# Optimization experiments

Measured on AMD Instinct MI355X. Metric: run time of the kernel, lower is better.

## Reference

```python
import jax, jax.numpy as jnp
import numpy as np

N, E, F, H, G, C, L = 50000, 800000, 128, 256, 128, 10, 3


def _gcn(x, src, dst, norm, W, b, n):
    # PyG GCNConv: h = x W; out_i = sum_{j->i} norm_ji h_j (+ self loops already in src/dst); + bias
    h = x @ W
    msg = h[src] * norm[:, None]              # [E+N, H]
    return jax.ops.segment_sum(msg, dst, num_segments=n) + b


def setup_inputs() -> dict:
    key = jax.random.key(0)
    ks = jax.random.split(key, 8)
    x = jax.random.normal(ks[0], (N, F), dtype=jnp.float32)
    edge_index = jax.random.randint(ks[1], (2, E), 0, N, dtype=jnp.int32)
    batch = jnp.sort(jax.random.randint(ks[2], (N,), 0, G, dtype=jnp.int32))
    graph_hidden = jax.random.normal(ks[3], (G, H), dtype=jnp.float32)
    W0 = jax.random.normal(ks[4], (F, H), dtype=jnp.float32) / np.sqrt(F)
    b0 = jnp.zeros((H,), jnp.float32)
    Ws = jax.random.normal(ks[5], (L, H, H), dtype=jnp.float32) / np.sqrt(H)
    bs = jnp.zeros((L, H), jnp.float32)
    Wlin = jax.random.normal(ks[6], (H, C), dtype=jnp.float32) / np.sqrt(H)
    blin = jnp.zeros((C,), jnp.float32)
    return {"x": x, "edge_index": edge_index, "batch": batch, "graph_hidden": graph_hidden,
            "W0": W0, "b0": b0, "Ws": Ws, "bs": bs, "Wlin": Wlin, "blin": blin}


def reference(x, edge_index, batch, graph_hidden, W0, b0, Ws, bs, Wlin, blin):
    n = x.shape[0]
    loops = jnp.arange(n, dtype=edge_index.dtype)
    src = jnp.concatenate([edge_index[0], loops])   # self loops appended
    dst = jnp.concatenate([edge_index[1], loops])
    deg = jax.ops.segment_sum(jnp.ones_like(src, dtype=x.dtype), dst, num_segments=n)
    inv_sqrt = jnp.where(deg > 0, jax.lax.rsqrt(deg), 0.0)
    norm = inv_sqrt[src] * inv_sqrt[dst]            # [E+N]

    h = _gcn(x, src, dst, norm, W0, b0, n)          # to_hidden (no activation, matches source)
    res = jax.lax.stop_gradient(graph_hidden[batch])  # no_grad residual, vectorized
    for i in range(Ws.shape[0]):
        h = h + res
        h = jax.nn.relu(_gcn(h, src, dst, norm, Ws[i], bs[i], n))
        # dropout is identity in eval mode

    counts = jax.ops.segment_sum(jnp.ones((n,), x.dtype), batch, num_segments=G)
    gm = jax.ops.segment_sum(h, batch, num_segments=G) / jnp.maximum(counts, 1.0)[:, None]
    gm = gm + graph_hidden
    y = gm @ Wlin + blin
    return (y, gm)
```

## Files before the change

kernel.cpp:

```cpp
#include <hip/hip_runtime.h>


typedef float f32x4 __attribute__((ext_vector_type(4)));
typedef float f32x2 __attribute__((ext_vector_type(2)));

__device__ inline float bf2f(unsigned short u) {
  union { unsigned int i; float f; } v;
  v.i = (unsigned int)u << 16;
  return v.f;
}
__device__ inline unsigned short f2bf(float f) {
  union { unsigned int i; float f; } v;
  v.f = f;
  unsigned int i = v.i;
  return (unsigned short)((i + 0x7fffu + ((i >> 16) & 1u)) >> 16);
}
__device__ inline unsigned pack4_fp8(float a, float b, float c, float d) {
  int r = 0;
  r = __builtin_amdgcn_cvt_pk_fp8_f32(a, b, r, false);
  r = __builtin_amdgcn_cvt_pk_fp8_f32(c, d, r, true);
  return (unsigned)r;
}
__device__ inline unsigned char f2fp8(float v) {
  return (unsigned char)((unsigned)__builtin_amdgcn_cvt_pk_fp8_f32(v, v, 0, false) & 0xffu);
}
__device__ inline void acc16_fp8(float* acc, uint4 r, unsigned msk) {
  unsigned w[4] = {r.x, r.y, r.z, r.w};
#pragma unroll
  for (int d = 0; d < 4; ++d) {
    int v = (int)(w[d] & msk);
    f32x2 lo = __builtin_amdgcn_cvt_pk_f32_fp8(v, false);
    f32x2 hi = __builtin_amdgcn_cvt_pk_f32_fp8(v, true);
    acc[4 * d + 0] += lo[0];
    acc[4 * d + 1] += lo[1];
    acc[4 * d + 2] += hi[0];
    acc[4 * d + 3] += hi[1];
  }
}
__device__ inline int lbound(const int* a, int n, int key) {
  int lo = 0, hi = n;
  while (lo < hi) {
    int mid = (lo + hi) >> 1;
    if (a[mid] < key) lo = mid + 1; else hi = mid;
  }
  return lo;
}


__global__ void count_pos_kernel(const int* __restrict__ dst, int* __restrict__ deg,
                                 unsigned char* __restrict__ pos, int E) {
  int t = blockIdx.x * blockDim.x + threadIdx.x;
  int e = t * 4;
  if (e + 3 < E) {
    int4 d4 = *(const int4*)&dst[e];
    uchar4 p4;
    p4.x = (unsigned char)atomicAdd(&deg[d4.x], 1);
    p4.y = (unsigned char)atomicAdd(&deg[d4.y], 1);
    p4.z = (unsigned char)atomicAdd(&deg[d4.z], 1);
    p4.w = (unsigned char)atomicAdd(&deg[d4.w], 1);
    *(uchar4*)&pos[e] = p4;
  } else {
    for (; e < E; ++e) pos[e] = (unsigned char)atomicAdd(&deg[dst[e]], 1);
  }
}

__global__ void scan_partial_kernel(const int* __restrict__ deg, float* __restrict__ inv_s,
                                    int* __restrict__ bsum, float* __restrict__ gmsum, int GH,
                                    int N) {
  __shared__ int s[256];
  int i = blockIdx.x * 256 + threadIdx.x;
  if (i < GH) gmsum[i] = 0.f;
  int d = (i < N) ? deg[i] : 0;
  if (i < N) inv_s[i] = rsqrtf((float)(d + 1));
  s[threadIdx.x] = d;
  __syncthreads();
  for (int off = 128; off > 0; off >>= 1) {
    if (threadIdx.x < off) s[threadIdx.x] += s[threadIdx.x + off];
    __syncthreads();
  }
  if (threadIdx.x == 0) bsum[blockIdx.x] = s[0];
}

__global__ void scan_final_kernel(const int* __restrict__ deg, const int* __restrict__ bsum,
                                  int* __restrict__ row_off, int NB, int N) {
  __shared__ int s[256];
  __shared__ int s2[256];
  int tid = threadIdx.x;
  int v2 = (tid < blockIdx.x && tid < NB) ? bsum[tid] : 0;
  s2[tid] = v2;
  __syncthreads();
  for (int off = 128; off > 0; off >>= 1) {
    if (tid < off) s2[tid] += s2[tid + off];
    __syncthreads();
  }
  int boff = s2[0];
  __syncthreads();
  int i = blockIdx.x * 256 + tid;
  int v = (i < N) ? deg[i] : 0;
  s[tid] = v;
  __syncthreads();
  for (int off = 1; off < 256; off <<= 1) {
    int t = (tid >= off) ? s[tid - off] : 0;
    __syncthreads();
    s[tid] += t;
    __syncthreads();
  }
  if (i < N) row_off[i] = boff + s[tid] - v;
  if (blockIdx.x == NB - 1 && tid == 255) row_off[N] = boff + s[255];
}

__global__ void fill_prep_kernel(const int* __restrict__ src, const int* __restrict__ dst,
                                 const unsigned char* __restrict__ pos,
                                 const int* __restrict__ row_off, int* __restrict__ col, int E,
                                 int FB, const float* __restrict__ x,
                                 const float* __restrict__ inv_s, unsigned* __restrict__ u,
                                 int total_dw, const float* __restrict__ W0,
                                 const float* __restrict__ Ws, unsigned char* __restrict__ Wt0,
                                 unsigned char* __restrict__ WtS) {
  const int FH = 128 * 256, HH = 256 * 256;
  int b = blockIdx.x;
  if (b < FB) {
    int t = b * 256 + threadIdx.x;
    int e = t * 4;
    if (e + 3 < E) {
      int4 s4 = *(const int4*)&src[e];
      int4 d4 = *(const int4*)&dst[e];
      uchar4 p4 = *(const uchar4*)&pos[e];
      col[row_off[d4.x] + p4.x] = s4.x;
      col[row_off[d4.y] + p4.y] = s4.y;
      col[row_off[d4.z] + p4.z] = s4.z;
      col[row_off[d4.w] + p4.w] = s4.w;
    } else {
      for (; e < E; ++e) col[row_off[dst[e]] + pos[e]] = src[e];
    }
  } else {
    int idx = (b - FB) * 256 + threadIdx.x;
    if (idx < total_dw) {
      int i = idx >> 5;
      float s = inv_s[i];
      float4 v = *(const float4*)&x[(size_t)idx * 4];
      u[idx] = pack4_fp8(s * v.x, s * v.y, s * v.z, s * v.w);
    } else {
      int w = idx - total_dw;
      if (w < FH) {
        int k = w >> 8, n = w & 255;
        Wt0[n * 128 + k] = f2fp8(W0[w]);
      } else {
        int t2 = w - FH;
        if (t2 < 3 * HH) {
          int l = t2 >> 16;
          int rem = t2 & 65535;
          int k = rem >> 8, n = rem & 255;
          WtS[l * HH + n * 256 + k] = f2fp8(Ws[t2]);
        }
      }
    }
  }
}

__global__ __launch_bounds__(256) void aggregate_fp8_ns128_kernel(
    const unsigned char* __restrict__ u, const int* __restrict__ row_off,
    const int* __restrict__ col, const float* __restrict__ inv_s,
    unsigned char* __restrict__ out, int N) {
  constexpr int CH = 128;
  int lane = threadIdx.x & 63;
  int wave = threadIdx.x >> 6;
  int grp = lane >> 3;
  int c = lane & 7;
  int i = blockIdx.x * 32 + wave * 8 + grp;
  if (i >= N) return;
  int e0 = row_off[i], e1 = row_off[i + 1];
  int last = e1 - 1;
  unsigned cofs = c * 16;
  float acc[16] = {};
  for (int e = e0; e < e1; e += 4) {
    unsigned off[4];
    unsigned msk[4];
#pragma unroll
    for (int q = 0; q < 4; ++q) {
      int ee = e + q;
      bool v = ee < e1;
      int j = col[v ? ee : last];
      off[q] = (unsigned)j * CH + cofs;
      msk[q] = v ? 0xffffffffu : 0u;
    }
    uint4 r[4];
#pragma unroll
    for (int q = 0; q < 4; ++q) r[q] = *(const uint4*)(u + off[q]);
#pragma unroll
    for (int q = 0; q < 4; ++q) acc16_fp8(acc, r[q], msk[q]);
  }
  uint4 self = *(const uint4*)(u + (size_t)i * CH + cofs);
  acc16_fp8(acc, self, 0xffffffffu);
  float s = inv_s[i];
  uint4 o;
  o.x = pack4_fp8(s * acc[0], s * acc[1], s * acc[2], s * acc[3]);
  o.y = pack4_fp8(s * acc[4], s * acc[5], s * acc[6], s * acc[7]);
  o.z = pack4_fp8(s * acc[8], s * acc[9], s * acc[10], s * acc[11]);
  o.w = pack4_fp8(s * acc[12], s * acc[13], s * acc[14], s * acc[15]);
  *(uint4*)(out + (size_t)i * CH + cofs) = o;
}

__global__ __launch_bounds__(256) void aggregate_fp8_ns_kernel(
    const unsigned char* __restrict__ u, const int* __restrict__ row_off,
    const int* __restrict__ col, const float* __restrict__ inv_s,
    unsigned char* __restrict__ out, int N) {
  constexpr int CH = 256;
  int slice = blockIdx.x & 1;
  int nb = blockIdx.x >> 1;
  int lane = threadIdx.x & 63;
  int wave = threadIdx.x >> 6;
  int grp = lane >> 3;
  int c = lane & 7;
  int i = nb * 32 + wave * 8 + grp;
  if (i >= N) return;
  int e0 = row_off[i], e1 = row_off[i + 1];
  int last = e1 - 1;
  unsigned sofs = (unsigned)slice * 128 + c * 16;
  float acc[16] = {};
  for (int e = e0; e < e1; e += 4) {
    unsigned off[4];
    unsigned msk[4];
#pragma unroll
    for (int q = 0; q < 4; ++q) {
      int ee = e + q;
      bool v = ee < e1;
      int j = col[v ? ee : last];
      off[q] = (unsigned)j * CH + sofs;
      msk[q] = v ? 0xffffffffu : 0u;
    }
    uint4 r[4];
#pragma unroll
    for (int q = 0; q < 4; ++q) r[q] = *(const uint4*)(u + off[q]);
#pragma unroll
    for (int q = 0; q < 4; ++q) acc16_fp8(acc, r[q], msk[q]);
  }
  uint4 self = *(const uint4*)(u + (size_t)i * CH + sofs);
  acc16_fp8(acc, self, 0xffffffffu);
  float s = inv_s[i];
  uint4 o;
  o.x = pack4_fp8(s * acc[0], s * acc[1], s * acc[2], s * acc[3]);
  o.y = pack4_fp8(s * acc[4], s * acc[5], s * acc[6], s * acc[7]);
  o.z = pack4_fp8(s * acc[8], s * acc[9], s * acc[10], s * acc[11]);
  o.w = pack4_fp8(s * acc[12], s * acc[13], s * acc[14], s * acc[15]);
  *(uint4*)(out + (size_t)i * CH + sofs) = o;
}

template <int K, bool RELU, int OUTMODE>
__global__ __launch_bounds__(512) void gemm_kernel(
    const unsigned char* __restrict__ A,
    const unsigned char* __restrict__ Bt,
    const float* __restrict__ bias,
    const float* __restrict__ inv_s, const int* __restrict__ batch,
    const float* __restrict__ gh,
    void* __restrict__ outp,
    int M) {
  constexpr int BK = 128;
  constexpr int LDT = 144;
  __shared__ unsigned char As[128 * LDT];
  __shared__ unsigned char Bs[256 * LDT];
  int tid = threadIdx.x;
  int wave = tid >> 6, lane = tid & 63;
  int quad = lane >> 4, l15 = lane & 15;
  int wr = wave >> 2, wc = wave & 3;
  int row0 = blockIdx.x * 128;
  f32x4 acc[4][4];
#pragma unroll
  for (int m = 0; m < 4; ++m)
#pragma unroll
    for (int n = 0; n < 4; ++n) acc[m][n] = (f32x4){0.f, 0.f, 0.f, 0.f};

  for (int k0 = 0; k0 < K; k0 += BK) {
#pragma unroll
    for (int p = 0; p < 2; ++p) {
      int uidx = tid + p * 512;
      int r = uidx >> 3, kq = uidx & 7;
      int gr = row0 + r;
      uint4 v = make_uint4(0u, 0u, 0u, 0u);
      if (gr < M) v = *(const uint4*)&A[(size_t)gr * K + k0 + kq * 16];
      *(uint4*)&As[r * LDT + kq * 16] = v;
    }
#pragma unroll
    for (int p = 0; p < 4; ++p) {
      int uidx = tid + p * 512;
      int n = uidx >> 3, kq = uidx & 7;
      *(uint4*)&Bs[n * LDT + kq * 16] = *(const uint4*)&Bt[(size_t)n * K + k0 + kq * 16];
    }
    __syncthreads();
#pragma unroll
    for (int s = 0; s < 4; ++s) {
      long long af[4], bfr[4];
#pragma unroll
      for (int m = 0; m < 4; ++m)
        af[m] = *(const long long*)&As[(wr * 64 + m * 16 + l15) * LDT + s * 32 + quad * 8];
#pragma unroll
      for (int n = 0; n < 4; ++n)
        bfr[n] = *(const long long*)&Bs[(wc * 64 + n * 16 + l15) * LDT + s * 32 + quad * 8];
#pragma unroll
      for (int m = 0; m < 4; ++m)
#pragma unroll
        for (int n = 0; n < 4; ++n)
          acc[m][n] =
              __builtin_amdgcn_mfma_f32_16x16x32_fp8_fp8(af[m], bfr[n], acc[m][n], 0, 0, 0);
    }
    if (k0 + BK < K) __syncthreads();
  }
  if (OUTMODE == 1) {
#pragma unroll
    for (int m = 0; m < 4; ++m) {
#pragma unroll
      for (int r = 0; r < 4; ++r) {
        int gr = row0 + wr * 64 + m * 16 + quad * 4 + r;
        if (gr >= M) continue;
        float sv = inv_s[gr];
        int bofs = batch[gr] * 256;
#pragma unroll
        for (int n = 0; n < 4; ++n) {
          int cc = wc * 64 + n * 16 + l15;
          float v = acc[m][n][r] + bias[cc];
          if (RELU) v = fmaxf(v, 0.f);
          v = sv * (v + gh[bofs + cc]);
          ((unsigned char*)outp)[(size_t)gr * 256 + cc] = f2fp8(v);
        }
      }
    }
  } else {
    float* gmsum = (float*)outp;
    float psum[4] = {0.f, 0.f, 0.f, 0.f};
    int cur_b = -1;
#pragma unroll
    for (int m = 0; m < 4; ++m) {
#pragma unroll
      for (int r = 0; r < 4; ++r) {
        int gr = row0 + wr * 64 + m * 16 + quad * 4 + r;
        if (gr >= M) continue;
        int b = batch[gr] * 256;
        if (b != cur_b) {
          if (cur_b >= 0) {
#pragma unroll
            for (int n = 0; n < 4; ++n)
              atomicAdd(&gmsum[cur_b + wc * 64 + n * 16 + l15], psum[n]);
          }
          cur_b = b;
#pragma unroll
          for (int n = 0; n < 4; ++n) psum[n] = 0.f;
        }
#pragma unroll
        for (int n = 0; n < 4; ++n) {
          int cc = wc * 64 + n * 16 + l15;
          float v = acc[m][n][r] + bias[cc];
          if (RELU) v = fmaxf(v, 0.f);
          psum[n] += v;
        }
      }
    }
    if (cur_b >= 0) {
#pragma unroll
      for (int n = 0; n < 4; ++n)
        atomicAdd(&gmsum[cur_b + wc * 64 + n * 16 + l15], psum[n]);
    }
  }
}


__global__ void final_kernel(const float* __restrict__ gmsum, const int* __restrict__ batch,
                             int N, const float* __restrict__ gh,
                             const float* __restrict__ Wlin, const float* __restrict__ blin,
                             float* __restrict__ y, float* __restrict__ gm_out, int G) {
  int g = blockIdx.x;
  int c = threadIdx.x;
  __shared__ float row[256];
  __shared__ int cnt_s;
  if (c == 0) cnt_s = lbound(batch, N, g + 1) - lbound(batch, N, g);
  __syncthreads();
  float v = gmsum[g * 256 + c] / fmaxf((float)cnt_s, 1.0f) + gh[g * 256 + c];
  gm_out[g * 256 + c] = v;
  row[c] = v;
  __syncthreads();
  if (c < 10) {
    float acc = blin[c];
    for (int k = 0; k < 256; ++k) acc += row[k] * Wlin[k * 10 + c];
    y[g * 10 + c] = acc;
  }
}


extern "C" void kernel_launch(void* const* d_in, const int* in_sizes, int n_in,
                              void* d_out, int out_size, void* d_ws, size_t ws_size,
                              hipStream_t stream) {
  const float* x = (const float*)d_in[0];
  const int* ei = (const int*)d_in[1];
  const int* batch = (const int*)d_in[2];
  const float* gh = (const float*)d_in[3];
  const float* W0 = (const float*)d_in[4];
  const float* b0 = (const float*)d_in[5];
  const float* Ws = (const float*)d_in[6];
  const float* bs = (const float*)d_in[7];
  const float* Wlin = (const float*)d_in[8];
  const float* blin = (const float*)d_in[9];
  float* out = (float*)d_out;

  const int N = in_sizes[2];
  const int E = in_sizes[1] / 2;
  const int G = in_sizes[3] / 256;
  const int H = 256, L = 3, C = 10, F = 128;

  char* ws = (char*)d_ws;
  size_t off = 0;
  auto alloc = [&](size_t bytes) {
    void* p = ws + off;
    off += (bytes + 255) & ~(size_t)255;
    return p;
  };
  int* deg = (int*)alloc((size_t)N * 4);
  float* gmsum = (float*)alloc((size_t)G * H * 4);
  int* row_off = (int*)alloc((size_t)(N + 1) * 4);
  int* bsum = (int*)alloc(256 * 4);
  int* col = (int*)alloc((size_t)E * 4);
  unsigned char* pos = (unsigned char*)alloc((size_t)E);
  float* inv_s = (float*)alloc((size_t)N * 4);
  unsigned char* u_x = (unsigned char*)alloc((size_t)N * F);
  unsigned char* uA = (unsigned char*)alloc((size_t)N * H);
  unsigned char* aggA = (unsigned char*)alloc((size_t)N * H);
  unsigned char* Wt0 = (unsigned char*)alloc((size_t)F * H);
  unsigned char* WtS = (unsigned char*)alloc((size_t)L * H * H);

  const int* srcv = ei;
  const int* dstv = ei + E;

  hipMemsetAsync(deg, 0, (size_t)N * 4, stream);

  int NB = (N + 255) / 256;
  int CPB = ((E + 3) / 4 + 255) / 256;
  count_pos_kernel<<<CPB, 256, 0, stream>>>(dstv, deg, pos, E);
  scan_partial_kernel<<<NB, 256, 0, stream>>>(deg, inv_s, bsum, gmsum, G * H, N);
  scan_final_kernel<<<NB, 256, 0, stream>>>(deg, bsum, row_off, NB, N);

  int FB = ((E + 3) / 4 + 255) / 256;
  int UXDW = N * (F / 4);
  int TW = F * H + 3 * H * H;
  int PREPB = (UXDW + TW + 255) / 256;
  fill_prep_kernel<<<FB + PREPB, 256, 0, stream>>>(srcv, dstv, pos, row_off, col, E, FB, x,
                                                   inv_s, (unsigned*)u_x, UXDW, W0, Ws, Wt0,
                                                   WtS);

  int AGG0_GRID = (N + 31) / 32;
  int AGG_NS_GRID = ((N + 31) / 32) * 2;
  int GEMM_GRID = (N + 127) / 128;

  aggregate_fp8_ns128_kernel<<<AGG0_GRID, 256, 0, stream>>>(u_x, row_off, col, inv_s, aggA, N);
  gemm_kernel<128, false, 1><<<GEMM_GRID, 512, 0, stream>>>(aggA, Wt0, b0, inv_s, batch, gh,
                                                            uA, N);
  for (int l = 0; l < 2; ++l) {
    aggregate_fp8_ns_kernel<<<AGG_NS_GRID, 256, 0, stream>>>(uA, row_off, col, inv_s, aggA, N);
    gemm_kernel<256, true, 1><<<GEMM_GRID, 512, 0, stream>>>(
        aggA, WtS + (size_t)l * H * H, bs + (size_t)l * H, inv_s, batch, gh, uA, N);
  }
  aggregate_fp8_ns_kernel<<<AGG_NS_GRID, 256, 0, stream>>>(uA, row_off, col, inv_s, aggA, N);
  gemm_kernel<256, true, 2><<<GEMM_GRID, 512, 0, stream>>>(
      aggA, WtS + (size_t)2 * H * H, bs + (size_t)2 * H, inv_s, batch, gh, gmsum, N);

  final_kernel<<<G, 256, 0, stream>>>(gmsum, batch, N, gh, Wlin, blin, out,
                                      out + (size_t)G * C, G);
}
```

Baseline: 346.5 us.

## Store fp8 node features in 64-byte column slices for gather locality

Node features are now written by the prep kernel and the GEMM epilogue as column-sliced planes, each holding 64 bytes per node, instead of full contiguous rows. The aggregation kernels process one slice per block, using 4 lanes per node and 64 nodes per block. Each gathered neighbour row becomes a single 64-byte segment, and the per-slice working set is smaller, which should improve cache hit rates in the gather-heavy SpMM. In exchange, the grid has more blocks that each re-read the CSR indices, and the GEMM epilogue's fp8 stores are more scattered.

After: 364.1 us. +5.1%, slower.

```diff
diff --git a/kernel.cpp b/kernel.cpp
--- a/kernel.cpp
+++ b/kernel.cpp
@@ -137,9 +137,14 @@
     int idx = (b - FB) * 256 + threadIdx.x;
     if (idx < total_dw) {
       int i = idx >> 5;
+      int q = idx & 31;
+      int slice = q >> 4;
+      int qq = q & 15;
       float s = inv_s[i];
       float4 v = *(const float4*)&x[(size_t)idx * 4];
-      u[idx] = pack4_fp8(s * v.x, s * v.y, s * v.z, s * v.w);
+      int Nn = total_dw >> 5;
+      u[(size_t)slice * Nn * 16 + (size_t)i * 16 + qq] =
+          pack4_fp8(s * v.x, s * v.y, s * v.z, s * v.w);
     } else {
       int w = idx - total_dw;
       if (w < FH) {
@@ -158,19 +163,21 @@
   }
 }
 
-__global__ __launch_bounds__(256) void aggregate_fp8_ns128_kernel(
+__global__ __launch_bounds__(256) void aggregate_fp8_sm2_kernel(
     const unsigned char* __restrict__ u, const int* __restrict__ row_off,
     const int* __restrict__ col, const float* __restrict__ inv_s,
     unsigned char* __restrict__ out, int N) {
-  constexpr int CH = 128;
+  int slice = blockIdx.x & 1;
+  int nb = blockIdx.x >> 1;
   int lane = threadIdx.x & 63;
   int wave = threadIdx.x >> 6;
-  int grp = lane >> 3;
-  int c = lane & 7;
-  int i = blockIdx.x * 32 + wave * 8 + grp;
+  int grp = lane >> 2;
+  int c = lane & 3;
+  int i = nb * 64 + wave * 16 + grp;
   if (i >= N) return;
   int e0 = row_off[i], e1 = row_off[i + 1];
   int last = e1 - 1;
+  const unsigned char* base = u + (size_t)slice * N * 64;
   unsigned cofs = c * 16;
   float acc[16] = {};
   for (int e = e0; e < e1; e += 4) {
@@ -181,16 +188,16 @@
       int ee = e + q;
       bool v = ee < e1;
       int j = col[v ? ee : last];
-      off[q] = (unsigned)j * CH + cofs;
+      off[q] = (unsigned)j * 64 + cofs;
       msk[q] = v ? 0xffffffffu : 0u;
     }
     uint4 r[4];
 #pragma unroll
-    for (int q = 0; q < 4; ++q) r[q] = *(const uint4*)(u + off[q]);
+    for (int q = 0; q < 4; ++q) r[q] = *(const uint4*)(base + off[q]);
 #pragma unroll
     for (int q = 0; q < 4; ++q) acc16_fp8(acc, r[q], msk[q]);
   }
-  uint4 self = *(const uint4*)(u + (size_t)i * CH + cofs);
+  uint4 self = *(const uint4*)(base + (size_t)i * 64 + cofs);
   acc16_fp8(acc, self, 0xffffffffu);
   float s = inv_s[i];
   uint4 o;
@@ -198,25 +205,25 @@
   o.y = pack4_fp8(s * acc[4], s * acc[5], s * acc[6], s * acc[7]);
   o.z = pack4_fp8(s * acc[8], s * acc[9], s * acc[10], s * acc[11]);
   o.w = pack4_fp8(s * acc[12], s * acc[13], s * acc[14], s * acc[15]);
-  *(uint4*)(out + (size_t)i * CH + cofs) = o;
-}
-
-__global__ __launch_bounds__(256) void aggregate_fp8_ns_kernel(
+  *(uint4*)(out + (size_t)i * 128 + slice * 64 + cofs) = o;
+}
+
+__global__ __launch_bounds__(256) void aggregate_fp8_sm4_kernel(
     const unsigned char* __restrict__ u, const int* __restrict__ row_off,
     const int* __restrict__ col, const float* __restrict__ inv_s,
     unsigned char* __restrict__ out, int N) {
-  constexpr int CH = 256;
-  int slice = blockIdx.x & 1;
-  int nb = blockIdx.x >> 1;
+  int slice = blockIdx.x & 3;
+  int nb = blockIdx.x >> 2;
   int lane = threadIdx.x & 63;
   int wave = threadIdx.x >> 6;
-  int grp = lane >> 3;
-  int c = lane & 7;
-  int i = nb * 32 + wave * 8 + grp;
+  int grp = lane >> 2;
+  int c = lane & 3;
+  int i = nb * 64 + wave * 16 + grp;
   if (i >= N) return;
   int e0 = row_off[i], e1 = row_off[i + 1];
   int last = e1 - 1;
-  unsigned sofs = (unsigned)slice * 128 + c * 16;
+  const unsigned char* base = u + (size_t)slice * N * 64;
+  unsigned cofs = c * 16;
   float acc[16] = {};
   for (int e = e0; e < e1; e += 4) {
     unsigned off[4];
@@ -226,16 +233,16 @@
       int ee = e + q;
       bool v = ee < e1;
       int j = col[v ? ee : last];
-      off[q] = (unsigned)j * CH + sofs;
+      off[q] = (unsigned)j * 64 + cofs;
       msk[q] = v ? 0xffffffffu : 0u;
     }
     uint4 r[4];
 #pragma unroll
-    for (int q = 0; q < 4; ++q) r[q] = *(const uint4*)(u + off[q]);
+    for (int q = 0; q < 4; ++q) r[q] = *(const uint4*)(base + off[q]);
 #pragma unroll
     for (int q = 0; q < 4; ++q) acc16_fp8(acc, r[q], msk[q]);
   }
-  uint4 self = *(const uint4*)(u + (size_t)i * CH + sofs);
+  uint4 self = *(const uint4*)(base + (size_t)i * 64 + cofs);
   acc16_fp8(acc, self, 0xffffffffu);
   float s = inv_s[i];
   uint4 o;
@@ -243,7 +250,7 @@
   o.y = pack4_fp8(s * acc[4], s * acc[5], s * acc[6], s * acc[7]);
   o.z = pack4_fp8(s * acc[8], s * acc[9], s * acc[10], s * acc[11]);
   o.w = pack4_fp8(s * acc[12], s * acc[13], s * acc[14], s * acc[15]);
-  *(uint4*)(out + (size_t)i * CH + sofs) = o;
+  *(uint4*)(out + (size_t)i * 256 + slice * 64 + cofs) = o;
 }
 
 template <int K, bool RELU, int OUTMODE>
@@ -306,6 +313,7 @@
     if (k0 + BK < K) __syncthreads();
   }
   if (OUTMODE == 1) {
+    unsigned char* u4 = (unsigned char*)outp;
 #pragma unroll
     for (int m = 0; m < 4; ++m) {
 #pragma unroll
@@ -320,7 +328,7 @@
           float v = acc[m][n][r] + bias[cc];
           if (RELU) v = fmaxf(v, 0.f);
           v = sv * (v + gh[bofs + cc]);
-          ((unsigned char*)outp)[(size_t)gr * 256 + cc] = f2fp8(v);
+          u4[(size_t)(cc >> 6) * M * 64 + (size_t)gr * 64 + (cc & 63)] = f2fp8(v);
         }
       }
     }
@@ -444,19 +452,19 @@
                                                    inv_s, (unsigned*)u_x, UXDW, W0, Ws, Wt0,
                                                    WtS);
 
-  int AGG0_GRID = (N + 31) / 32;
-  int AGG_NS_GRID = ((N + 31) / 32) * 2;
+  int AGG2_GRID = ((N + 63) / 64) * 2;
+  int AGG4_GRID = ((N + 63) / 64) * 4;
   int GEMM_GRID = (N + 127) / 128;
 
-  aggregate_fp8_ns128_kernel<<<AGG0_GRID, 256, 0, stream>>>(u_x, row_off, col, inv_s, aggA, N);
+  aggregate_fp8_sm2_kernel<<<AGG2_GRID, 256, 0, stream>>>(u_x, row_off, col, inv_s, aggA, N);
   gemm_kernel<128, false, 1><<<GEMM_GRID, 512, 0, stream>>>(aggA, Wt0, b0, inv_s, batch, gh,
                                                             uA, N);
   for (int l = 0; l < 2; ++l) {
-    aggregate_fp8_ns_kernel<<<AGG_NS_GRID, 256, 0, stream>>>(uA, row_off, col, inv_s, aggA, N);
+    aggregate_fp8_sm4_kernel<<<AGG4_GRID, 256, 0, stream>>>(uA, row_off, col, inv_s, aggA, N);
     gemm_kernel<256, true, 1><<<GEMM_GRID, 512, 0, stream>>>(
         aggA, WtS + (size_t)l * H * H, bs + (size_t)l * H, inv_s, batch, gh, uA, N);
   }
-  aggregate_fp8_ns_kernel<<<AGG_NS_GRID, 256, 0, stream>>>(uA, row_off, col, inv_s, aggA, N);
+  aggregate_fp8_sm4_kernel<<<AGG4_GRID, 256, 0, stream>>>(uA, row_off, col, inv_s, aggA, N);
   gemm_kernel<256, true, 2><<<GEMM_GRID, 512, 0, stream>>>(
       aggA, WtS + (size_t)2 * H * H, bs + (size_t)2 * H, inv_s, batch, gh, gmsum, N);
 
```
